# Optimization experiments

Hardware: AMD Instinct MI355X
Metric: run time of the kernel (lower is better)

## Reference

```python
import jax, jax.numpy as jnp
import numpy as np

B, N, K, DIM = 8, 2048, 8, 128
EPS = 1e-5  # BatchNorm eps (torch default); BN evaluated in inference mode with running stats


def _xavier(key, o, i):
    lim = float(np.sqrt(6.0 / (i + o)))
    return jax.random.uniform(key, (o, i), jnp.float32, -lim, lim)


def setup_inputs() -> dict:
    key = jax.random.key(0)
    ks = jax.random.split(key, 8)
    x = jax.random.normal(ks[0], (B, 3, N), jnp.float32)
    w0 = _xavier(ks[1], DIM, 3)
    b0 = jnp.zeros((DIM,), jnp.float32)
    ws = jnp.stack([_xavier(ks[2 + i], DIM, DIM) for i in range(2)])  # [2,DIM,DIM]
    bs = jnp.zeros((2, DIM), jnp.float32)
    # BatchNorm (eval-mode) params / running stats, mildly randomized so math is exercised
    bn_g = 1.0 + 0.1 * jax.random.normal(ks[4], (3, DIM), jnp.float32)
    bn_b = 0.1 * jax.random.normal(ks[5], (3, DIM), jnp.float32)
    bn_m = 0.1 * jax.random.normal(ks[6], (3, DIM), jnp.float32)
    bn_v = jax.random.uniform(ks[7], (3, DIM), jnp.float32, 0.5, 1.5)
    return {"x": x, "w0": w0, "b0": b0, "ws": ws, "bs": bs,
            "bn_g": bn_g, "bn_b": bn_b, "bn_m": bn_m, "bn_v": bn_v}


def _group(x):
    # x: [B,3,N] -> relative kNN coords [B,3,N,K] (torch code uses [B,3,K,N]; axis order
    # is immaterial since the MLP is pointwise and the max is over the neighbor axis)
    inner = jnp.einsum('bcn,bcm->bnm', x, x)
    sq = jnp.sum(x * x, axis=1)                      # [B,N]
    dist = sq[:, :, None] - 2.0 * inner + sq[:, None, :]
    idx = jax.lax.top_k(-dist, K)[1]                 # [B,N,K] nearest (incl. self)
    grouped = jax.vmap(lambda xi, ii: xi[:, ii])(x, idx)  # [B,3,N,K]
    return grouped - x[:, :, :, None]


def _block(h, w, b, g, be, m, v):
    # 1x1 conv + eval-mode BatchNorm + ReLU over channel axis 1
    h = jnp.einsum('oc,bcnk->bonk', w, h) + b[None, :, None, None]
    scale = (g / jnp.sqrt(v + EPS))[None, :, None, None]
    h = (h - m[None, :, None, None]) * scale + be[None, :, None, None]
    return jax.nn.relu(h)


def reference(x, w0, b0, ws, bs, bn_g, bn_b, bn_m, bn_v):
    h = _group(x)                                    # [B,3,N,K]
    h = _block(h, w0, b0, bn_g[0], bn_b[0], bn_m[0], bn_v[0])
    for i in range(2):
        h = _block(h, ws[i], bs[i], bn_g[i + 1], bn_b[i + 1], bn_m[i + 1], bn_v[i + 1])
    return jnp.max(h, axis=3)                        # [B,DIM,N]
```

## Files before the change

### kernel.cpp

```cpp
#include <hip/hip_runtime.h>


#define EPSF 1e-5f
#define FMAXV 3.402823466e+38f

#define NB 8
#define NN 2048
#define KNBR 8
#define DIMF 128
#define NQ (NB * NN)
#define NPAIR (NQ * KNBR)

#define OFF16_W1H 0
#define OFF16_W1L 16384
#define OFF16_W2H 32768
#define OFF16_W2L 49152
#define OFF_C0 32768
#define OFF_C1 32896
#define OFF_C2 33024
#define OFF_Y 33792
#define OFF_IDX (OFF_Y + NQ * DIMF)

typedef __attribute__((ext_vector_type(4))) float f32x4;
typedef __attribute__((ext_vector_type(8))) short short8v;

__device__ __forceinline__ float relu_f(float a) { return fmaxf(a, 0.0f); }

__device__ __forceinline__ void split3(float f, unsigned& hi, unsigned& lo) {
  const unsigned u = __float_as_uint(f);
  const unsigned h = (u + 0x7FFFu + ((u >> 16) & 1u)) >> 16;
  const float hf = __uint_as_float(h << 16);
  lo = __float_as_uint(f - hf) >> 16;
  hi = h;
}

__device__ __forceinline__ f32x4 mfma16x16x32bf(short8v a, short8v b, f32x4 c) {
  return __builtin_amdgcn_mfma_f32_16x16x32_bf16(a, b, c, 0, 0, 0);
}

#define KCSWAP(a, b)                  \
  {                                   \
    const float mn_ = fminf(a, b);    \
    const float mx_ = fmaxf(a, b);    \
    (a) = mn_; (b) = mx_;             \
  }

#define SORT8(d0, d1, d2, d3, d4, d5, d6, d7)                   \
  KCSWAP(d0, d1) KCSWAP(d2, d3) KCSWAP(d4, d5) KCSWAP(d6, d7)   \
  KCSWAP(d0, d2) KCSWAP(d1, d3) KCSWAP(d4, d6) KCSWAP(d5, d7)   \
  KCSWAP(d1, d2) KCSWAP(d5, d6)                                 \
  KCSWAP(d0, d4) KCSWAP(d1, d5) KCSWAP(d2, d6) KCSWAP(d3, d7)   \
  KCSWAP(d2, d4) KCSWAP(d3, d5)                                 \
  KCSWAP(d1, d2) KCSWAP(d3, d4) KCSWAP(d5, d6)

#define KCLEAN8()                                               \
  KCSWAP(k0, k4) KCSWAP(k1, k5) KCSWAP(k2, k6) KCSWAP(k3, k7)   \
  KCSWAP(k0, k2) KCSWAP(k1, k3) KCSWAP(k4, k6) KCSWAP(k5, k7)   \
  KCSWAP(k0, k1) KCSWAP(k2, k3) KCSWAP(k4, k5) KCSWAP(k6, k7)

#define KFOLD8(d0, d1, d2, d3, d4, d5, d6, d7)                  \
  {                                                             \
    k0 = fminf(k0, d7); k1 = fminf(k1, d6);                     \
    k2 = fminf(k2, d5); k3 = fminf(k3, d4);                     \
    k4 = fminf(k4, d3); k5 = fminf(k5, d2);                     \
    k6 = fminf(k6, d1); k7 = fminf(k7, d0);                     \
    KCLEAN8()                                                   \
  }

#define KMERGE(mv)                                              \
  {                                                             \
    const float q0_ = __shfl_xor(k0, mv, 64);                   \
    const float q1_ = __shfl_xor(k1, mv, 64);                   \
    const float q2_ = __shfl_xor(k2, mv, 64);                   \
    const float q3_ = __shfl_xor(k3, mv, 64);                   \
    const float q4_ = __shfl_xor(k4, mv, 64);                   \
    const float q5_ = __shfl_xor(k5, mv, 64);                   \
    const float q6_ = __shfl_xor(k6, mv, 64);                   \
    const float q7_ = __shfl_xor(k7, mv, 64);                   \
    k0 = fminf(k0, q7_); k1 = fminf(k1, q6_);                   \
    k2 = fminf(k2, q5_); k3 = fminf(k3, q4_);                   \
    k4 = fminf(k4, q3_); k5 = fminf(k5, q2_);                   \
    k6 = fminf(k6, q1_); k7 = fminf(k7, q0_);                   \
    KCLEAN8()                                                   \
  }

__global__ __launch_bounds__(512, 4) void knn_kernel(
    const float* __restrict__ x, const float* __restrict__ w0,
    const float* __restrict__ b0, const float* __restrict__ wstk,
    const float* __restrict__ bstk, const float* __restrict__ g,
    const float* __restrict__ be, const float* __restrict__ bm,
    const float* __restrict__ bv, float* __restrict__ ws) {
  __shared__ float2 xyp[2080];
  __shared__ float2 zsp[2080];
  const int t = threadIdx.x;
  const int bid = blockIdx.x;

  if (bid >= 1024) {
    const int i = (bid - 1024) * 512 + t;
    unsigned short* __restrict__ wsh = (unsigned short*)ws;
    const int fo = i >> 7, k = i & 127;
    const float s1 = g[128 + fo] / sqrtf(bv[128 + fo] + EPSF);
    const float s2 = g[256 + fo] / sqrtf(bv[256 + fo] + EPSF);
    unsigned h1, l1, h2, l2;
    split3(wstk[i] * s1, h1, l1);
    split3(wstk[16384 + i] * s2, h2, l2);
    const int dst = ((fo >> 4) * 4 + (k >> 5)) * 512 +
                    (((k >> 3) & 3) * 16 + (fo & 15)) * 8 + (k & 7);
    wsh[OFF16_W1H + dst] = (unsigned short)h1;
    wsh[OFF16_W1L + dst] = (unsigned short)l1;
    wsh[OFF16_W2H + dst] = (unsigned short)h2;
    wsh[OFF16_W2L + dst] = (unsigned short)l2;
    if (bid == 1024 && t < 128) {
      const int f = t;
      const float s0 = g[f] / sqrtf(bv[f] + EPSF);
      const float s1b = g[128 + f] / sqrtf(bv[128 + f] + EPSF);
      const float s2b = g[256 + f] / sqrtf(bv[256 + f] + EPSF);
      ws[OFF_C0 + f] = (b0[f] - bm[f]) * s0 + be[f];
      ws[OFF_C1 + f] = (bstk[f] - bm[128 + f]) * s1b + be[128 + f];
      ws[OFF_C2 + f] = (bstk[128 + f] - bm[256 + f]) * s2b + be[256 + f];
    }
    return;
  }

  const int bb = bid >> 7;
  const int qloc0 = (bid & 127) * 16;
  const float* __restrict__ xb = x + bb * 3 * NN;

#pragma unroll
  for (int k = 0; k < 4; ++k) {
    const int i = t + k * 512;
    const float a0 = xb[i];
    const float a1 = xb[2048 + i];
    const float a2 = xb[4096 + i];
    const float sq = fmaf(a2, a2, fmaf(a1, a1, a0 * a0));
    const int ii = i + (i >> 6);
    xyp[ii] = make_float2(a0, a1);
    zsp[ii] = make_float2(a2, sq);
  }

  const int qi = t >> 5;
  const int sg = t & 31;
  const int n = qloc0 + qi;
  const int q = bb * NN + n;
  const float qx0 = xb[n], qx1 = xb[2048 + n], qx2 = xb[4096 + n];
  const float sqn = fmaf(qx2, qx2, fmaf(qx1, qx1, qx0 * qx0));

  {
    const int f0 = sg * 4;
    float4 yv;
    {
      const float s0 = g[f0] / sqrtf(bv[f0] + EPSF);
      yv.x = fmaf(w0[3 * f0 + 2] * s0, qx2,
                  fmaf(w0[3 * f0 + 1] * s0, qx1, (w0[3 * f0] * s0) * qx0));
    }
    {
      const float s0 = g[f0 + 1] / sqrtf(bv[f0 + 1] + EPSF);
      yv.y = fmaf(w0[3 * f0 + 5] * s0, qx2,
                  fmaf(w0[3 * f0 + 4] * s0, qx1, (w0[3 * f0 + 3] * s0) * qx0));
    }
    {
      const float s0 = g[f0 + 2] / sqrtf(bv[f0 + 2] + EPSF);
      yv.z = fmaf(w0[3 * f0 + 8] * s0, qx2,
                  fmaf(w0[3 * f0 + 7] * s0, qx1, (w0[3 * f0 + 6] * s0) * qx0));
    }
    {
      const float s0 = g[f0 + 3] / sqrtf(bv[f0 + 3] + EPSF);
      yv.w = fmaf(w0[3 * f0 + 11] * s0, qx2,
                  fmaf(w0[3 * f0 + 10] * s0, qx1, (w0[3 * f0 + 9] * s0) * qx0));
    }
    *(float4*)(ws + OFF_Y + (long)q * 128 + f0) = yv;
  }
  __syncthreads();

  const float2* __restrict__ xr = xyp + sg * 65;
  const float2* __restrict__ zr = zsp + sg * 65;

  float dv[64];
  float k0 = FMAXV, k1 = FMAXV, k2 = FMAXV, k3 = FMAXV,
        k4 = FMAXV, k5 = FMAXV, k6 = FMAXV, k7 = FMAXV;
#pragma unroll
  for (int bt = 0; bt < 8; ++bt) {
    float d0, d1, d2, d3, d4, d5, d6, d7;
#define KD(j, dj)                                                        \
    {                                                                    \
      const float2 cxy = xr[bt * 8 + (j)];                               \
      const float2 czs = zr[bt * 8 + (j)];                               \
      const float inner =                                                \
          fmaf(qx2, czs.x, fmaf(qx1, cxy.y, qx0 * cxy.x));               \
      dj = (sqn - 2.0f * inner) + czs.y;                                 \
    }
    KD(0, d0) KD(1, d1) KD(2, d2) KD(3, d3)
    KD(4, d4) KD(5, d5) KD(6, d6) KD(7, d7)
#undef KD
    dv[bt * 8 + 0] = d0; dv[bt * 8 + 1] = d1;
    dv[bt * 8 + 2] = d2; dv[bt * 8 + 3] = d3;
    dv[bt * 8 + 4] = d4; dv[bt * 8 + 5] = d5;
    dv[bt * 8 + 6] = d6; dv[bt * 8 + 7] = d7;
    SORT8(d0, d1, d2, d3, d4, d5, d6, d7)
    KFOLD8(d0, d1, d2, d3, d4, d5, d6, d7)
  }

  KMERGE(1) KMERGE(2) KMERGE(4) KMERGE(8) KMERGE(16)
  const float thr = k7;

  unsigned am = 0, bm2 = 0;
#pragma unroll
  for (int mm = 0; mm < 32; ++mm) am |= (dv[mm] <= thr) ? (1u << mm) : 0u;
#pragma unroll
  for (int mm = 0; mm < 32; ++mm)
    bm2 |= (dv[32 + mm] <= thr) ? (1u << mm) : 0u;

  const int cnt = __popc(am) + __popc(bm2);
  int inc = cnt, tq;
  tq = __shfl_up(inc, 1, 32); inc += (sg >= 1) ? tq : 0;
  tq = __shfl_up(inc, 2, 32); inc += (sg >= 2) ? tq : 0;
  tq = __shfl_up(inc, 4, 32); inc += (sg >= 4) ? tq : 0;
  tq = __shfl_up(inc, 8, 32); inc += (sg >= 8) ? tq : 0;
  tq = __shfl_up(inc, 16, 32); inc += (sg >= 16) ? tq : 0;
  int pos = inc - cnt;

  int* __restrict__ idxg = (int*)(ws + OFF_IDX);
  {
    unsigned w = am;
    while (w) {
      const int b = __ffs(w) - 1;
      w &= w - 1;
      if (pos < 8) idxg[q * 8 + pos] = bb * NN + sg * 64 + b;
      ++pos;
    }
    w = bm2;
    while (w) {
      const int b = __ffs(w) - 1;
      w &= w - 1;
      if (pos < 8) idxg[q * 8 + pos] = bb * NN + sg * 64 + 32 + b;
      ++pos;
    }
  }
}

__global__ __launch_bounds__(256, 2) void fused_kernel(float* __restrict__ ws,
                                                       float* __restrict__ out) {
  extern __shared__ char smem[];
  unsigned* __restrict__ H = (unsigned*)(smem + 32768);
  float* __restrict__ OS = (float*)(smem + 49152);

  const float* __restrict__ y = ws + OFF_Y;
  const int* __restrict__ idxg = (const int*)(ws + OFF_IDX);
  const unsigned short* __restrict__ wsu = (const unsigned short*)ws;

  const int t = threadIdx.x;
  const int lane = t & 63, w = t >> 6;
  const int wc = w;
  const int bid = blockIdx.x;
  const int bb = bid & 7, qseg = bid >> 3;
  const int chunk0 = bb * 512 + qseg * 8;

  short8v w1h[2][4], w1l[2][4], w2h[2][4], w2l[2][4];
#pragma unroll
  for (int ft = 0; ft < 2; ++ft)
#pragma unroll
    for (int ks = 0; ks < 4; ++ks) {
      const int off = ((wc * 2 + ft) * 4 + ks) * 512 + lane * 8;
      w1h[ft][ks] = *(const short8v*)(wsu + OFF16_W1H + off);
      w1l[ft][ks] = *(const short8v*)(wsu + OFF16_W1L + off);
      w2h[ft][ks] = *(const short8v*)(wsu + OFF16_W2H + off);
      w2l[ft][ks] = *(const short8v*)(wsu + OFF16_W2L + off);
    }

  const float c1v0 = (ws + OFF_C1)[wc * 32 + (lane & 15)];
  const float c1v1 = (ws + OFF_C1)[wc * 32 + 16 + (lane & 15)];
  const float c2v0 = (ws + OFF_C2)[wc * 32 + (lane & 15)];
  const float c2v1 = (ws + OFF_C2)[wc * 32 + 16 + (lane & 15)];

  const int row = t >> 3, part8 = t & 7;
  const float* __restrict__ c0p = ws + OFF_C0 + part8 * 16;
  const float4 c0a = *(const float4*)(c0p + 0);
  const float4 c0b = *(const float4*)(c0p + 4);
  const float4 c0c = *(const float4*)(c0p + 8);
  const float4 c0d = *(const float4*)(c0p + 12);

#define PACK_WRITE_A(base, hv, kc)                              \
  {                                                             \
    unsigned hh[8], ll[8];                                      \
    _Pragma("unroll") for (int e = 0; e < 8; ++e)               \
        split3(hv[e], hh[e], ll[e]);                            \
    int4 hp, lp;                                                \
    hp.x = (int)(hh[0] | (hh[1] << 16));                        \
    hp.y = (int)(hh[2] | (hh[3] << 16));                        \
    hp.z = (int)(hh[4] | (hh[5] << 16));                        \
    hp.w = (int)(hh[6] | (hh[7] << 16));                        \
    lp.x = (int)(ll[0] | (ll[1] << 16));                        \
    lp.y = (int)(ll[2] | (ll[3] << 16));                        \
    lp.z = (int)(ll[4] | (ll[5] << 16));                        \
    lp.w = (int)(ll[6] | (ll[7] << 16));                        \
    const int col = (kc) ^ (row & 7);                           \
    *(int4*)((base) + row * 256 + col * 16) = hp;               \
    *(int4*)((base) + 8192 + row * 256 + col * 16) = lp;        \
  }

  {
    const int gp = chunk0 * 32 + row;
    const int mg = idxg[gp];
    const float* __restrict__ ym = y + (long)mg * 128 + part8 * 16;
    const float* __restrict__ yn = y + (long)(gp >> 3) * 128 + part8 * 16;
    const float4 a0 = *(const float4*)(ym + 0);
    const float4 a1 = *(const float4*)(ym + 4);
    const float4 a2 = *(const float4*)(ym + 8);
    const float4 a3 = *(const float4*)(ym + 12);
    const float4 n0 = *(const float4*)(yn + 0);
    const float4 n1 = *(const float4*)(yn + 4);
    const float4 n2 = *(const float4*)(yn + 8);
    const float4 n3 = *(const float4*)(yn + 12);
    float hv0[8] = {relu_f(a0.x - n0.x + c0a.x), relu_f(a0.y - n0.y + c0a.y),
                    relu_f(a0.z - n0.z + c0a.z), relu_f(a0.w - n0.w + c0a.w),
                    relu_f(a1.x - n1.x + c0b.x), relu_f(a1.y - n1.y + c0b.y),
                    relu_f(a1.z - n1.z + c0b.z), relu_f(a1.w - n1.w + c0b.w)};
    float hv1[8] = {relu_f(a2.x - n2.x + c0c.x), relu_f(a2.y - n2.y + c0c.y),
                    relu_f(a2.z - n2.z + c0c.z), relu_f(a2.w - n2.w + c0c.w),
                    relu_f(a3.x - n3.x + c0d.x), relu_f(a3.y - n3.y + c0d.y),
                    relu_f(a3.z - n3.z + c0d.z), relu_f(a3.w - n3.w + c0d.w)};
    PACK_WRITE_A(smem, hv0, part8 * 2)
    PACK_WRITE_A(smem, hv1, part8 * 2 + 1)
  }
  __syncthreads();

#pragma unroll 1
  for (int j = 0; j < 8; ++j) {
    char* __restrict__ Acur = smem + (j & 1) * 16384;
    char* __restrict__ Anxt = smem + ((j & 1) ^ 1) * 16384;

    int mg_next = 0, gp_next = 0;
    if (j < 7) {
      gp_next = (chunk0 + j + 1) * 32 + row;
      mg_next = idxg[gp_next];
    }

    f32x4 acc[2][2];
#pragma unroll
    for (int pt = 0; pt < 2; ++pt)
#pragma unroll
      for (int ft = 0; ft < 2; ++ft) acc[pt][ft] = (f32x4){0.f, 0.f, 0.f, 0.f};
#pragma unroll
    for (int ks = 0; ks < 4; ++ks) {
      const int kc = ks * 4 + (lane >> 4);
#pragma unroll
      for (int pt = 0; pt < 2; ++pt) {
        const int arow = pt * 16 + (lane & 15);
        const int col = kc ^ (arow & 7);
        const short8v ah = *(const short8v*)(Acur + arow * 256 + col * 16);
        const short8v al =
            *(const short8v*)(Acur + 8192 + arow * 256 + col * 16);
#pragma unroll
        for (int ft = 0; ft < 2; ++ft) {
          acc[pt][ft] = mfma16x16x32bf(al, w1h[ft][ks], acc[pt][ft]);
          acc[pt][ft] = mfma16x16x32bf(ah, w1l[ft][ks], acc[pt][ft]);
          acc[pt][ft] = mfma16x16x32bf(ah, w1h[ft][ks], acc[pt][ft]);
        }
      }
    }

    float4 a0, a1, a2, a3, n0, n1, n2, n3;
    if (j < 7) {
      const float* __restrict__ ym = y + (long)mg_next * 128 + part8 * 16;
      const float* __restrict__ yn = y + (long)(gp_next >> 3) * 128 + part8 * 16;
      a0 = *(const float4*)(ym + 0);
      a1 = *(const float4*)(ym + 4);
      a2 = *(const float4*)(ym + 8);
      a3 = *(const float4*)(ym + 12);
      n0 = *(const float4*)(yn + 0);
      n1 = *(const float4*)(yn + 4);
      n2 = *(const float4*)(yn + 8);
      n3 = *(const float4*)(yn + 12);
    }

#pragma unroll
    for (int pt = 0; pt < 2; ++pt)
#pragma unroll
      for (int ft = 0; ft < 2; ++ft) {
        const int fo = wc * 32 + ft * 16 + (lane & 15);
        const int cc = fo >> 2;
        const float cb = ft ? c1v1 : c1v0;
#pragma unroll
        for (int reg = 0; reg < 4; ++reg) {
          const int p = pt * 16 + (lane >> 4) * 4 + reg;
          const float vv = relu_f(acc[pt][ft][reg] + cb);
          unsigned hh, ll;
          split3(vv, hh, ll);
          H[p * 128 + ((cc ^ (p & 7)) << 2) + (fo & 3)] = (hh << 16) | ll;
        }
      }
    __syncthreads();

    f32x4 acc2[2][2];
#pragma unroll
    for (int pt = 0; pt < 2; ++pt)
#pragma unroll
      for (int ft = 0; ft < 2; ++ft) acc2[pt][ft] = (f32x4){0.f, 0.f, 0.f, 0.f};
#pragma unroll
    for (int ks = 0; ks < 4; ++ks) {
      const int cc0 = ks * 8 + (lane >> 4) * 2;
#pragma unroll
      for (int pt = 0; pt < 2; ++pt) {
        const int p = pt * 16 + (lane & 15);
        const int4 u0 = *(const int4*)&H[p * 128 + ((cc0 ^ (p & 7)) << 2)];
        const int4 u1 = *(const int4*)&H[p * 128 + (((cc0 + 1) ^ (p & 7)) << 2)];
        const unsigned uu[8] = {(unsigned)u0.x, (unsigned)u0.y, (unsigned)u0.z,
                                (unsigned)u0.w, (unsigned)u1.x, (unsigned)u1.y,
                                (unsigned)u1.z, (unsigned)u1.w};
        short8v ah, al;
#pragma unroll
        for (int e = 0; e < 8; ++e) {
          ah[e] = (short)(uu[e] >> 16);
          al[e] = (short)(uu[e] & 0xFFFFu);
        }
#pragma unroll
        for (int ft = 0; ft < 2; ++ft) {
          acc2[pt][ft] = mfma16x16x32bf(al, w2h[ft][ks], acc2[pt][ft]);
          acc2[pt][ft] = mfma16x16x32bf(ah, w2l[ft][ks], acc2[pt][ft]);
          acc2[pt][ft] = mfma16x16x32bf(ah, w2h[ft][ks], acc2[pt][ft]);
        }
      }
    }
    __syncthreads();

    {
      const int g = lane >> 4;
#pragma unroll
      for (int pt = 0; pt < 2; ++pt)
#pragma unroll
        for (int ft = 0; ft < 2; ++ft) {
          const int fo = wc * 32 + ft * 16 + (lane & 15);
          const float cb = ft ? c2v1 : c2v0;
          const float v0 = relu_f(acc2[pt][ft][0] + cb);
          const float v1 = relu_f(acc2[pt][ft][1] + cb);
          const float v2 = relu_f(acc2[pt][ft][2] + cb);
          const float v3 = relu_f(acc2[pt][ft][3] + cb);
          float m = fmaxf(fmaxf(v0, v1), fmaxf(v2, v3));
          m = fmaxf(m, __shfl_xor(m, 16, 64));
          if ((g & 1) == 0) {
            const int qloc = pt * 2 + (g >> 1);
            OS[(j * 4 + qloc) * 128 + fo] = m;
          }
        }
    }

    if (j < 7) {
      float hv0[8] = {relu_f(a0.x - n0.x + c0a.x), relu_f(a0.y - n0.y + c0a.y),
                      relu_f(a0.z - n0.z + c0a.z), relu_f(a0.w - n0.w + c0a.w),
                      relu_f(a1.x - n1.x + c0b.x), relu_f(a1.y - n1.y + c0b.y),
                      relu_f(a1.z - n1.z + c0b.z), relu_f(a1.w - n1.w + c0b.w)};
      float hv1[8] = {relu_f(a2.x - n2.x + c0c.x), relu_f(a2.y - n2.y + c0c.y),
                      relu_f(a2.z - n2.z + c0c.z), relu_f(a2.w - n2.w + c0c.w),
                      relu_f(a3.x - n3.x + c0d.x), relu_f(a3.y - n3.y + c0d.y),
                      relu_f(a3.z - n3.z + c0d.z), relu_f(a3.w - n3.w + c0d.w)};
      PACK_WRITE_A(Anxt, hv0, part8 * 2)
      PACK_WRITE_A(Anxt, hv1, part8 * 2 + 1)
    }
    __syncthreads();
  }

  {
    const int f = t >> 1, seg = t & 1;
    float* __restrict__ op =
        out + (long)(bb * 128 + f) * 2048 + qseg * 32 + seg * 16;
#pragma unroll
    for (int u = 0; u < 4; ++u) {
      float4 o;
      o.x = OS[(seg * 16 + u * 4 + 0) * 128 + f];
      o.y = OS[(seg * 16 + u * 4 + 1) * 128 + f];
      o.z = OS[(seg * 16 + u * 4 + 2) * 128 + f];
      o.w = OS[(seg * 16 + u * 4 + 3) * 128 + f];
      *(float4*)(op + u * 4) = o;
    }
  }
}

extern "C" void kernel_launch(void* const* d_in, const int* in_sizes, int n_in,
                              void* d_out, int out_size, void* d_ws,
                              size_t ws_size, hipStream_t stream) {
  (void)in_sizes; (void)n_in; (void)out_size; (void)ws_size;
  const float* x = (const float*)d_in[0];
  const float* w0 = (const float*)d_in[1];
  const float* b0 = (const float*)d_in[2];
  const float* wst = (const float*)d_in[3];
  const float* bst = (const float*)d_in[4];
  const float* g = (const float*)d_in[5];
  const float* be = (const float*)d_in[6];
  const float* bm = (const float*)d_in[7];
  const float* bv = (const float*)d_in[8];
  float* out = (float*)d_out;
  float* ws = (float*)d_ws;

  hipFuncSetAttribute((const void*)fused_kernel,
                      hipFuncAttributeMaxDynamicSharedMemorySize, 65536);

  knn_kernel<<<1056, 512, 0, stream>>>(x, w0, b0, wst, bst, g, be, bm, bv, ws);
  fused_kernel<<<512, 256, 65536, stream>>>(ws, out);
}
```

Measured before the change: 67.10 us.

## Recompute layer-0 features from raw coordinates instead of gathering precomputed Y

The kNN kernel no longer writes a per-point 128-channel layer-0 projection Y to global memory. Instead, the fused kernel gathers the neighbor's and query's xyz, forms the relative vector, and recomputes the 3->128 conv+BN layer from BN-folded weights staged in LDS. This cuts a 8MB write plus heavy 512-byte-per-neighbor gathers in exchange for a few FMAs per channel. It also adds s_setprio around the MFMA loops, and grows LDS per block by 2KB, which may affect occupancy.

```diff
diff --git a/kernel.cpp b/kernel.cpp
--- a/kernel.cpp
+++ b/kernel.cpp
@@ -15,11 +15,10 @@
 #define OFF16_W1L 16384
 #define OFF16_W2H 32768
 #define OFF16_W2L 49152
-#define OFF_C0 32768
 #define OFF_C1 32896
 #define OFF_C2 33024
-#define OFF_Y 33792
-#define OFF_IDX (OFF_Y + NQ * DIMF)
+#define OFF_W0F 33152
+#define OFF_IDX 33792
 
 typedef __attribute__((ext_vector_type(4))) float f32x4;
 typedef __attribute__((ext_vector_type(8))) short short8v;
@@ -115,9 +114,14 @@
       const float s0 = g[f] / sqrtf(bv[f] + EPSF);
       const float s1b = g[128 + f] / sqrtf(bv[128 + f] + EPSF);
       const float s2b = g[256 + f] / sqrtf(bv[256 + f] + EPSF);
-      ws[OFF_C0 + f] = (b0[f] - bm[f]) * s0 + be[f];
       ws[OFF_C1 + f] = (bstk[f] - bm[128 + f]) * s1b + be[128 + f];
       ws[OFF_C2 + f] = (bstk[128 + f] - bm[256 + f]) * s2b + be[256 + f];
+      float4 wv;
+      wv.x = w0[3 * f + 0] * s0;
+      wv.y = w0[3 * f + 1] * s0;
+      wv.z = w0[3 * f + 2] * s0;
+      wv.w = (b0[f] - bm[f]) * s0 + be[f];
+      *((float4*)(ws + OFF_W0F) + f) = wv;
     }
     return;
   }
@@ -144,32 +148,6 @@
   const int q = bb * NN + n;
   const float qx0 = xb[n], qx1 = xb[2048 + n], qx2 = xb[4096 + n];
   const float sqn = fmaf(qx2, qx2, fmaf(qx1, qx1, qx0 * qx0));
-
-  {
-    const int f0 = sg * 4;
-    float4 yv;
-    {
-      const float s0 = g[f0] / sqrtf(bv[f0] + EPSF);
-      yv.x = fmaf(w0[3 * f0 + 2] * s0, qx2,
-                  fmaf(w0[3 * f0 + 1] * s0, qx1, (w0[3 * f0] * s0) * qx0));
-    }
-    {
-      const float s0 = g[f0 + 1] / sqrtf(bv[f0 + 1] + EPSF);
-      yv.y = fmaf(w0[3 * f0 + 5] * s0, qx2,
-                  fmaf(w0[3 * f0 + 4] * s0, qx1, (w0[3 * f0 + 3] * s0) * qx0));
-    }
-    {
-      const float s0 = g[f0 + 2] / sqrtf(bv[f0 + 2] + EPSF);
-      yv.z = fmaf(w0[3 * f0 + 8] * s0, qx2,
-                  fmaf(w0[3 * f0 + 7] * s0, qx1, (w0[3 * f0 + 6] * s0) * qx0));
-    }
-    {
-      const float s0 = g[f0 + 3] / sqrtf(bv[f0 + 3] + EPSF);
-      yv.w = fmaf(w0[3 * f0 + 11] * s0, qx2,
-                  fmaf(w0[3 * f0 + 10] * s0, qx1, (w0[3 * f0 + 9] * s0) * qx0));
-    }
-    *(float4*)(ws + OFF_Y + (long)q * 128 + f0) = yv;
-  }
   __syncthreads();
 
   const float2* __restrict__ xr = xyp + sg * 65;
@@ -238,13 +216,14 @@
   }
 }
 
-__global__ __launch_bounds__(256, 2) void fused_kernel(float* __restrict__ ws,
-                                                       float* __restrict__ out) {
+__global__ __launch_bounds__(256, 2) void fused_kernel(
+    const float* __restrict__ x, float* __restrict__ ws,
+    float* __restrict__ out) {
   extern __shared__ char smem[];
   unsigned* __restrict__ H = (unsigned*)(smem + 32768);
   float* __restrict__ OS = (float*)(smem + 49152);
-
-  const float* __restrict__ y = ws + OFF_Y;
+  float4* __restrict__ W0L = (float4*)(smem + 65536);
+
   const int* __restrict__ idxg = (const int*)(ws + OFF_IDX);
   const unsigned short* __restrict__ wsu = (const unsigned short*)ws;
 
@@ -254,6 +233,12 @@
   const int bid = blockIdx.x;
   const int bb = bid & 7, qseg = bid >> 3;
   const int chunk0 = bb * 512 + qseg * 8;
+  const float* __restrict__ xb = x + bb * 3 * NN;
+
+  if (t < 128) {
+    const float4 wv = *((const float4*)(ws + OFF_W0F) + t);
+    W0L[((t & 7) << 4) | (t >> 3)] = wv;
+  }
 
   short8v w1h[2][4], w1l[2][4], w2h[2][4], w2l[2][4];
 #pragma unroll
@@ -273,11 +258,7 @@
   const float c2v1 = (ws + OFF_C2)[wc * 32 + 16 + (lane & 15)];
 
   const int row = t >> 3, part8 = t & 7;
-  const float* __restrict__ c0p = ws + OFF_C0 + part8 * 16;
-  const float4 c0a = *(const float4*)(c0p + 0);
-  const float4 c0b = *(const float4*)(c0p + 4);
-  const float4 c0c = *(const float4*)(c0p + 8);
-  const float4 c0d = *(const float4*)(c0p + 12);
+  __syncthreads();
 
 #define PACK_WRITE_A(base, hv, kc)                              \
   {                                                             \
@@ -298,29 +279,29 @@
     *(int4*)((base) + 8192 + row * 256 + col * 16) = lp;        \
   }
 
+#define STAGE_A(base, R0, R1, R2)                               \
+  {                                                             \
+    float hv0[8], hv1[8];                                       \
+    _Pragma("unroll") for (int e = 0; e < 8; ++e) {             \
+      const float4 wa = W0L[e * 16 + part8 * 2];                \
+      const float4 wb = W0L[e * 16 + part8 * 2 + 1];            \
+      hv0[e] = relu_f(                                          \
+          fmaf(wa.z, R2, fmaf(wa.y, R1, fmaf(wa.x, R0, wa.w))));\
+      hv1[e] = relu_f(                                          \
+          fmaf(wb.z, R2, fmaf(wb.y, R1, fmaf(wb.x, R0, wb.w))));\
+    }                                                           \
+    PACK_WRITE_A(base, hv0, part8 * 2)                          \
+    PACK_WRITE_A(base, hv1, part8 * 2 + 1)                      \
+  }
+
   {
     const int gp = chunk0 * 32 + row;
     const int mg = idxg[gp];
-    const float* __restrict__ ym = y + (long)mg * 128 + part8 * 16;
-    const float* __restrict__ yn = y + (long)(gp >> 3) * 128 + part8 * 16;
-    const float4 a0 = *(const float4*)(ym + 0);
-    const float4 a1 = *(const float4*)(ym + 4);
-    const float4 a2 = *(const float4*)(ym + 8);
-    const float4 a3 = *(const float4*)(ym + 12);
-    const float4 n0 = *(const float4*)(yn + 0);
-    const float4 n1 = *(const float4*)(yn + 4);
-    const float4 n2 = *(const float4*)(yn + 8);
-    const float4 n3 = *(const float4*)(yn + 12);
-    float hv0[8] = {relu_f(a0.x - n0.x + c0a.x), relu_f(a0.y - n0.y + c0a.y),
-                    relu_f(a0.z - n0.z + c0a.z), relu_f(a0.w - n0.w + c0a.w),
-                    relu_f(a1.x - n1.x + c0b.x), relu_f(a1.y - n1.y + c0b.y),
-                    relu_f(a1.z - n1.z + c0b.z), relu_f(a1.w - n1.w + c0b.w)};
-    float hv1[8] = {relu_f(a2.x - n2.x + c0c.x), relu_f(a2.y - n2.y + c0c.y),
-                    relu_f(a2.z - n2.z + c0c.z), relu_f(a2.w - n2.w + c0c.w),
-                    relu_f(a3.x - n3.x + c0d.x), relu_f(a3.y - n3.y + c0d.y),
-                    relu_f(a3.z - n3.z + c0d.z), relu_f(a3.w - n3.w + c0d.w)};
-    PACK_WRITE_A(smem, hv0, part8 * 2)
-    PACK_WRITE_A(smem, hv1, part8 * 2 + 1)
+    const int mloc = mg & 2047, nloc = (gp >> 3) & 2047;
+    const float r0 = xb[mloc] - xb[nloc];
+    const float r1 = xb[2048 + mloc] - xb[2048 + nloc];
+    const float r2 = xb[4096 + mloc] - xb[4096 + nloc];
+    STAGE_A(smem, r0, r1, r2)
   }
   __syncthreads();
 
@@ -340,6 +321,7 @@
     for (int pt = 0; pt < 2; ++pt)
 #pragma unroll
       for (int ft = 0; ft < 2; ++ft) acc[pt][ft] = (f32x4){0.f, 0.f, 0.f, 0.f};
+    __builtin_amdgcn_s_setprio(1);
 #pragma unroll
     for (int ks = 0; ks < 4; ++ks) {
       const int kc = ks * 4 + (lane >> 4);
@@ -358,19 +340,14 @@
         }
       }
     }
-
-    float4 a0, a1, a2, a3, n0, n1, n2, n3;
+    __builtin_amdgcn_s_setprio(0);
+
+    float r0n = 0.f, r1n = 0.f, r2n = 0.f;
     if (j < 7) {
-      const float* __restrict__ ym = y + (long)mg_next * 128 + part8 * 16;
-      const float* __restrict__ yn = y + (long)(gp_next >> 3) * 128 + part8 * 16;
-      a0 = *(const float4*)(ym + 0);
-      a1 = *(const float4*)(ym + 4);
-      a2 = *(const float4*)(ym + 8);
-      a3 = *(const float4*)(ym + 12);
-      n0 = *(const float4*)(yn + 0);
-      n1 = *(const float4*)(yn + 4);
-      n2 = *(const float4*)(yn + 8);
-      n3 = *(const float4*)(yn + 12);
+      const int mloc = mg_next & 2047, nloc = (gp_next >> 3) & 2047;
+      r0n = xb[mloc] - xb[nloc];
+      r1n = xb[2048 + mloc] - xb[2048 + nloc];
+      r2n = xb[4096 + mloc] - xb[4096 + nloc];
     }
 
 #pragma unroll
@@ -396,6 +373,7 @@
     for (int pt = 0; pt < 2; ++pt)
 #pragma unroll
       for (int ft = 0; ft < 2; ++ft) acc2[pt][ft] = (f32x4){0.f, 0.f, 0.f, 0.f};
+    __builtin_amdgcn_s_setprio(1);
 #pragma unroll
     for (int ks = 0; ks < 4; ++ks) {
       const int cc0 = ks * 8 + (lane >> 4) * 2;
@@ -421,6 +399,7 @@
         }
       }
     }
+    __builtin_amdgcn_s_setprio(0);
     __syncthreads();
 
     {
@@ -445,16 +424,7 @@
     }
 
     if (j < 7) {
-      float hv0[8] = {relu_f(a0.x - n0.x + c0a.x), relu_f(a0.y - n0.y + c0a.y),
-                      relu_f(a0.z - n0.z + c0a.z), relu_f(a0.w - n0.w + c0a.w),
-                      relu_f(a1.x - n1.x + c0b.x), relu_f(a1.y - n1.y + c0b.y),
-                      relu_f(a1.z - n1.z + c0b.z), relu_f(a1.w - n1.w + c0b.w)};
-      float hv1[8] = {relu_f(a2.x - n2.x + c0c.x), relu_f(a2.y - n2.y + c0c.y),
-                      relu_f(a2.z - n2.z + c0c.z), relu_f(a2.w - n2.w + c0c.w),
-                      relu_f(a3.x - n3.x + c0d.x), relu_f(a3.y - n3.y + c0d.y),
-                      relu_f(a3.z - n3.z + c0d.z), relu_f(a3.w - n3.w + c0d.w)};
-      PACK_WRITE_A(Anxt, hv0, part8 * 2)
-      PACK_WRITE_A(Anxt, hv1, part8 * 2 + 1)
+      STAGE_A(Anxt, r0n, r1n, r2n)
     }
     __syncthreads();
   }
@@ -492,8 +462,8 @@
   float* ws = (float*)d_ws;
 
   hipFuncSetAttribute((const void*)fused_kernel,
-                      hipFuncAttributeMaxDynamicSharedMemorySize, 65536);
+                      hipFuncAttributeMaxDynamicSharedMemorySize, 69632);
 
   knn_kernel<<<1056, 512, 0, stream>>>(x, w0, b0, wst, bst, g, be, bm, bv, ws);
-  fused_kernel<<<512, 256, 65536, stream>>>(ws, out);
+  fused_kernel<<<512, 256, 67584, stream>>>(x, ws, out);
 }
```

New measurement: 60.90 us. 9.3% less time.
